# Optimization experiments

Hardware: AMD Instinct MI355X
Metric: run time of the kernel (lower is better)

The kernel has to match this reference:

```python
import jax, jax.numpy as jnp
import numpy as np

DIM = 768
HEADS = 12
E = 8
TOPK = 2
EPS = 1e-5


def layer_norm(x, g, b):
    m = jnp.mean(x, axis=-1, keepdims=True)
    v = jnp.mean((x - m) ** 2, axis=-1, keepdims=True)
    return (x - m) * jax.lax.rsqrt(v + EPS) * g + b


def setup_inputs() -> dict:
    key = jax.random.key(0)
    ks = jax.random.split(key, 12)
    B, N, C = 16, 1024, DIM
    s = 0.02
    return {
        "x": jax.random.normal(ks[0], (B, N, C), jnp.float32),
        "noise": jax.random.normal(ks[1], (B, N, E), jnp.float32),
        "ln1_g": jnp.ones((C,), jnp.float32),
        "ln1_b": jnp.zeros((C,), jnp.float32),
        "qkv_w": jax.random.normal(ks[2], (C, 3 * C), jnp.float32) * s,  # pre-transposed
        "proj_w": jax.random.normal(ks[3], (C, C), jnp.float32) * s,
        "proj_b": jnp.zeros((C,), jnp.float32),
        "ln2_g": jnp.ones((C,), jnp.float32),
        "ln2_b": jnp.zeros((C,), jnp.float32),
        "route_w": jax.random.normal(ks[4], (C, E), jnp.float32) * s,
        "route_b": jnp.zeros((E,), jnp.float32),
        "rln_g": jnp.ones((E,), jnp.float32),
        "rln_b": jnp.zeros((E,), jnp.float32),
        "expert_w": jax.random.normal(ks[5], (E, C, C), jnp.float32) * s,  # [E, in, out]
        "expert_b": jnp.zeros((E, C), jnp.float32),
    }


def reference(x, noise, ln1_g, ln1_b, qkv_w, proj_w, proj_b, ln2_g, ln2_b,
              route_w, route_b, rln_g, rln_b, expert_w, expert_b):
    B, N, C = x.shape
    H = HEADS
    Dh = C // H
    scale = Dh ** -0.5

    # --- Attention branch ---
    h = layer_norm(x, ln1_g, ln1_b)
    qkv = (h @ qkv_w).reshape(B, N, 3, H, Dh)
    q, k, v = qkv[:, :, 0], qkv[:, :, 1], qkv[:, :, 2]  # [B,N,H,Dh]
    attn = jnp.einsum('bnhd,bmhd->bhnm', q, k) * scale
    attn = jax.nn.softmax(attn, axis=-1)
    o = jnp.einsum('bhnm,bmhd->bnhd', attn, v).reshape(B, N, C)
    x = x + o @ proj_w + proj_b

    # --- MoE branch ---
    h = layer_norm(x, ln2_g, ln2_b)
    logits = layer_norm(h @ route_w + route_b, rln_g, rln_b)  # [B,N,E]
    rw = jax.nn.softmax(logits, axis=-1) + noise * (1.0 / E)
    topk_w, topk_idx = jax.lax.top_k(rw, TOPK)               # [B,N,K]
    topk_w = jax.nn.softmax(topk_w, axis=-1)

    # dense all-expert compute (faithful to source): [B,N,E,C]
    expert_out = jnp.einsum('bnc,ecd->bned', h, expert_w) + expert_b
    selected = jnp.take_along_axis(expert_out, topk_idx[..., None], axis=2)  # [B,N,K,C]
    moe = jnp.sum(selected * topk_w[..., None], axis=2)
    return x + moe
```

## Files before the change

kernel.cpp:

```cpp
#include <hip/hip_runtime.h>
#include <hip/hip_fp16.h>

typedef unsigned short u16;
typedef unsigned int u32;
typedef _Float16 f16;
typedef short bf16x8 __attribute__((ext_vector_type(8)));
typedef f16 f16x8 __attribute__((ext_vector_type(8)));
typedef float f32x4 __attribute__((ext_vector_type(4)));
typedef u32 u32x4 __attribute__((ext_vector_type(4)));

#define TOKENS 16384
#define CDIM 768
#define NEXP 8

#define QSCALE 0.18033688011112043f

__device__ __forceinline__ u16 f2b(float f) {
  u32 u = __float_as_uint(f);
  return (u16)((u + 0x7fffu + ((u >> 16) & 1u)) >> 16);
}
__device__ __forceinline__ u16 f16bits(f16 x) {
  union { f16 f; u16 u; } c;
  c.f = x;
  return c.u;
}
__device__ __forceinline__ f32x4 mfma_bf(bf16x8 a, bf16x8 b, f32x4 c) {
  return __builtin_amdgcn_mfma_f32_16x16x32_bf16(a, b, c, 0, 0, 0);
}
__device__ __forceinline__ f32x4 mfma_h(f16x8 a, f16x8 b, f32x4 c) {
  return __builtin_amdgcn_mfma_f32_16x16x32_f16(a, b, c, 0, 0, 0);
}
__device__ __forceinline__ void split8(const float* v, f16x8& h, f16x8& l) {
#pragma unroll
  for (int i = 0; i < 8; i++) {
    const f16 hh = (f16)v[i];
    h[i] = hh;
    l[i] = (f16)(v[i] - (float)hh);
  }
}

__global__ __launch_bounds__(256) void transpose_split_f16(
    const float* __restrict__ in, f16* __restrict__ oh, f16* __restrict__ ol,
    int K, int N) {
  __shared__ float tile[64][65];
  const int n0 = blockIdx.x * 64, k0 = blockIdx.y * 64;
#pragma unroll
  for (int i = 0; i < 16; i++) {
    const int s = threadIdx.x + i * 256;
    const int r = s >> 6, c = s & 63;
    tile[r][c] = in[(size_t)(k0 + r) * N + n0 + c];
  }
  __syncthreads();
#pragma unroll
  for (int i = 0; i < 16; i++) {
    const int s = threadIdx.x + i * 256;
    const int r = s >> 6, c = s & 63;
    const float v = tile[c][r];
    const f16 h = (f16)v;
    oh[(size_t)(n0 + r) * K + k0 + c] = h;
    ol[(size_t)(n0 + r) * K + k0 + c] = (f16)(v - (float)h);
  }
}

__global__ __launch_bounds__(256) void transpose_f32_bf16(
    const float* __restrict__ in, u16* __restrict__ out, int K, int N) {
  __shared__ u16 tile[64][65];
  const int z = blockIdx.z;
  in += (size_t)z * K * N;
  out += (size_t)z * K * N;
  const int n0 = blockIdx.x * 64, k0 = blockIdx.y * 64;
#pragma unroll
  for (int i = 0; i < 16; i++) {
    const int s = threadIdx.x + i * 256;
    const int r = s >> 6, c = s & 63;
    tile[r][c] = f2b(in[(size_t)(k0 + r) * N + n0 + c]);
  }
  __syncthreads();
#pragma unroll
  for (int i = 0; i < 16; i++) {
    const int s = threadIdx.x + i * 256;
    const int r = s >> 6, c = s & 63;
    out[(size_t)(n0 + r) * K + k0 + c] = tile[c][r];
  }
}

template <bool BF16OUT>
__global__ __launch_bounds__(256) void ln_rows(const float* __restrict__ in,
                                               const float* __restrict__ g,
                                               const float* __restrict__ bt,
                                               void* __restrict__ out) {
  const int row = blockIdx.x * 4 + (threadIdx.x >> 6);
  const int lane = threadIdx.x & 63;
  const size_t base = (size_t)row * CDIM;
  float v[12];
  float s = 0.f, ss = 0.f;
#pragma unroll
  for (int j = 0; j < 12; j++) {
    const int idx = lane + j * 64;
    v[j] = in[base + idx];
    s += v[j];
    ss += v[j] * v[j];
  }
#pragma unroll
  for (int m = 1; m < 64; m <<= 1) {
    s += __shfl_xor(s, m);
    ss += __shfl_xor(ss, m);
  }
  const float mean = s * (1.f / CDIM);
  const float var = ss * (1.f / CDIM) - mean * mean;
  const float rs = rsqrtf(var + 1e-5f);
#pragma unroll
  for (int j = 0; j < 12; j++) {
    const int idx = lane + j * 64;
    const float y = (v[j] - mean) * rs * g[idx] + bt[idx];
    if (BF16OUT)
      ((u16*)out)[base + idx] = f2b(y);
    else
      ((float*)out)[base + idx] = y;
  }
}

__global__ __launch_bounds__(256) void ln_rows_split(
    const float* __restrict__ in, const float* __restrict__ g,
    const float* __restrict__ bt, f16* __restrict__ oh,
    f16* __restrict__ ol) {
  const int row = blockIdx.x * 4 + (threadIdx.x >> 6);
  const int lane = threadIdx.x & 63;
  const size_t base = (size_t)row * CDIM;
  float v[12];
  float s = 0.f, ss = 0.f;
#pragma unroll
  for (int j = 0; j < 12; j++) {
    const int idx = lane + j * 64;
    v[j] = in[base + idx];
    s += v[j];
    ss += v[j] * v[j];
  }
#pragma unroll
  for (int m = 1; m < 64; m <<= 1) {
    s += __shfl_xor(s, m);
    ss += __shfl_xor(ss, m);
  }
  const float mean = s * (1.f / CDIM);
  const float var = ss * (1.f / CDIM) - mean * mean;
  const float rs = rsqrtf(var + 1e-5f);
#pragma unroll
  for (int j = 0; j < 12; j++) {
    const int idx = lane + j * 64;
    const float y = (v[j] - mean) * rs * g[idx] + bt[idx];
    const f16 hh = (f16)y;
    oh[base + idx] = hh;
    ol[base + idx] = (f16)(y - (float)hh);
  }
}

template <int EPI, bool ASPLIT>
__global__ __launch_bounds__(256) void gemm_f16s(
    const float* __restrict__ A, const f16* __restrict__ Ath,
    const f16* __restrict__ Atl, const f16* __restrict__ Bth,
    const f16* __restrict__ Btl, float* __restrict__ C, int M, int N, int K,
    const float* __restrict__ bias, const float* __restrict__ xres,
    f16* __restrict__ Oh, f16* __restrict__ Ol, u32* __restrict__ Ov) {
  __shared__ f16 Ah[128 * 64];
  __shared__ f16 Al[128 * 64];
  __shared__ f16 Bh[128 * 64];
  __shared__ f16 Bl[128 * 64];
  const int tid = threadIdx.x;
  const int lane = tid & 63, wv = tid >> 6;
  const int wr = wv >> 1, wc = wv & 1;
  const int lm = lane & 15, lq = lane >> 4;
  const int m0 = blockIdx.y * 128, n0 = blockIdx.x * 128;
  f32x4 acc[4][4];
  const f32x4 z4 = {0.f, 0.f, 0.f, 0.f};
#pragma unroll
  for (int i = 0; i < 4; i++)
#pragma unroll
    for (int j = 0; j < 4; j++) acc[i][j] = z4;

  for (int k0 = 0; k0 < K; k0 += 64) {
    __syncthreads();
#pragma unroll
    for (int i = 0; i < 4; i++) {
      const int s = tid + i * 256;
      const int r = s >> 3, g = s & 7;
      const int sw = r * 64 + ((g ^ (r & 7)) << 3);
      if constexpr (ASPLIT) {
        *(f16x8*)(&Ah[sw]) =
            *(const f16x8*)(Ath + (size_t)(m0 + r) * K + k0 + g * 8);
        *(f16x8*)(&Al[sw]) =
            *(const f16x8*)(Atl + (size_t)(m0 + r) * K + k0 + g * 8);
      } else {
        float av[8];
        *(float4*)&av[0] =
            *(const float4*)(A + (size_t)(m0 + r) * K + k0 + g * 8);
        *(float4*)&av[4] =
            *(const float4*)(A + (size_t)(m0 + r) * K + k0 + g * 8 + 4);
        f16x8 hh, ll;
        split8(av, hh, ll);
        *(f16x8*)(&Ah[sw]) = hh;
        *(f16x8*)(&Al[sw]) = ll;
      }
      *(f16x8*)(&Bh[sw]) = *(const f16x8*)(Bth + (size_t)(n0 + r) * K + k0 + g * 8);
      *(f16x8*)(&Bl[sw]) = *(const f16x8*)(Btl + (size_t)(n0 + r) * K + k0 + g * 8);
    }
    __syncthreads();
#pragma unroll
    for (int kx = 0; kx < 8; kx += 4) {
      f16x8 afh[4], afl[4], bfh[4], bfl[4];
#pragma unroll
      for (int i = 0; i < 4; i++) {
        const int ra = wr * 64 + i * 16 + lm;
        const int aw = ra * 64 + (((ra & 7) ^ (kx + lq)) << 3);
        afh[i] = *(const f16x8*)(&Ah[aw]);
        afl[i] = *(const f16x8*)(&Al[aw]);
        const int rb = wc * 64 + i * 16 + lm;
        const int bw = rb * 64 + (((rb & 7) ^ (kx + lq)) << 3);
        bfh[i] = *(const f16x8*)(&Bh[bw]);
        bfl[i] = *(const f16x8*)(&Bl[bw]);
      }
#pragma unroll
      for (int i = 0; i < 4; i++)
#pragma unroll
        for (int j = 0; j < 4; j++) {
          acc[i][j] = mfma_h(afh[i], bfh[j], acc[i][j]);
          acc[i][j] = mfma_h(afh[i], bfl[j], acc[i][j]);
          acc[i][j] = mfma_h(afl[i], bfh[j], acc[i][j]);
        }
    }
  }
#pragma unroll
  for (int i = 0; i < 4; i++)
#pragma unroll
    for (int r = 0; r < 4; r++) {
      const size_t row = m0 + wr * 64 + i * 16 + lq * 4 + r;
#pragma unroll
      for (int j = 0; j < 4; j++) {
        const int col = n0 + wc * 64 + j * 16 + lm;
        float v = acc[i][j][r];
        if constexpr (EPI == 0) {
          C[row * N + col] = v;
        } else if constexpr (EPI == 1) {
          v += bias[col] + xres[row * N + col];
          C[row * N + col] = v;
        } else {
          if (n0 < 768) v *= QSCALE;
          const f16 hh = (f16)v;
          const f16 ll = (f16)(v - (float)hh);
          if (n0 < 1536) {
            Oh[row * 1536 + col] = hh;
            Ol[row * 1536 + col] = ll;
          } else {
            Ov[row * 768 + (col - 1536)] =
                (u32)f16bits(hh) | ((u32)f16bits(ll) << 16);
          }
        }
      }
    }
}

__global__ __launch_bounds__(256) void attn_f16s(
    const f16* __restrict__ qkh, const f16* __restrict__ qkl,
    const u32* __restrict__ vI, f16* __restrict__ oh, f16* __restrict__ ol,
    int qb) {
  __shared__ f16 Kh[64 * 64];
  __shared__ f16 Kl[64 * 64];
  __shared__ f16 Vh[64 * 64];
  __shared__ f16 Vl[64 * 64];
  __shared__ f16 Ph[4 * 16 * 64];
  __shared__ f16 Pl[4 * 16 * 64];
  const int bz = blockIdx.z, h = blockIdx.y, qt = blockIdx.x;
  const int tid = threadIdx.x, wv = tid >> 6, lane = tid & 63;
  const int lm = lane & 15, lq = lane >> 4;

  f16x8 qh[2], ql[2];
  {
    const size_t qrow =
        (size_t)(bz * 1024 + qt * 64 + wv * 16 + lm) * 1536 + h * 64;
#pragma unroll
    for (int f = 0; f < 2; f++) {
      qh[f] = *(const f16x8*)(qkh + qrow + f * 32 + lq * 8);
      ql[f] = *(const f16x8*)(qkl + qrow + f * 32 + lq * 8);
    }
  }
  const f32x4 z4 = {0.f, 0.f, 0.f, 0.f};
  f32x4 oacc[4];
#pragma unroll
  for (int jb = 0; jb < 4; jb++) oacc[jb] = z4;
  float mrun[4], lrun[4];
#pragma unroll
  for (int r = 0; r < 4; r++) {
    mrun[r] = -1e30f;
    lrun[r] = 0.f;
  }
  const int vd = tid & 63;
  const int vkg = tid >> 6;
  f16* pwh = &Ph[wv * 16 * 64];
  f16* pwl = &Pl[wv * 16 * 64];

  for (int kt = 0; kt < 16; kt++) {
    __syncthreads();
#pragma unroll
    for (int i = 0; i < 2; i++) {
      const int s2 = tid + i * 256;
      const int r = s2 >> 3, g = s2 & 7;
      const size_t kb =
          (size_t)(bz * 1024 + kt * 64 + r) * 1536 + 768 + h * 64 + g * 8;
      const int sw = r * 64 + ((g ^ (r & 7)) << 3);
      *(f16x8*)(&Kh[sw]) = *(const f16x8*)(qkh + kb);
      *(f16x8*)(&Kl[sw]) = *(const f16x8*)(qkl + kb);
    }
#pragma unroll
    for (int sseg = 0; sseg < 2; sseg++) {
      const int k0v = vkg * 16 + sseg * 8;
      f16x8 hh, ll;
#pragma unroll
      for (int j = 0; j < 8; j++) {
        const u32 w = vI[(size_t)(bz * 1024 + kt * 64 + k0v + j) * 768 +
                         h * 64 + vd];
        ((u16*)&hh)[j] = (u16)(w & 0xffffu);
        ((u16*)&ll)[j] = (u16)(w >> 16);
      }
      const int g = k0v >> 3;
      const int sw = vd * 64 + ((g ^ (vd & 7)) << 3);
      *(f16x8*)(&Vh[sw]) = hh;
      *(f16x8*)(&Vl[sw]) = ll;
    }
    __syncthreads();

    f32x4 sa[4];
#pragma unroll
    for (int j = 0; j < 4; j++) sa[j] = z4;
#pragma unroll
    for (int kx = 0; kx < 8; kx += 4) {
      const f16x8 ah = qh[kx >> 2], al = ql[kx >> 2];
#pragma unroll
      for (int j = 0; j < 4; j++) {
        const int rb = j * 16 + lm;
        const int bw = rb * 64 + (((rb & 7) ^ (kx + lq)) << 3);
        const f16x8 bh = *(const f16x8*)(&Kh[bw]);
        const f16x8 bl = *(const f16x8*)(&Kl[bw]);
        sa[j] = mfma_h(ah, bh, sa[j]);
        sa[j] = mfma_h(ah, bl, sa[j]);
        sa[j] = mfma_h(al, bh, sa[j]);
      }
    }

#pragma unroll
    for (int r = 0; r < 4; r++) {
      float mx = fmaxf(fmaxf(sa[0][r], sa[1][r]), fmaxf(sa[2][r], sa[3][r]));
      mx = fmaxf(mx, __shfl_xor(mx, 1));
      mx = fmaxf(mx, __shfl_xor(mx, 2));
      mx = fmaxf(mx, __shfl_xor(mx, 4));
      mx = fmaxf(mx, __shfl_xor(mx, 8));
      const float mnew = fmaxf(mrun[r], mx);
      const float alpha = exp2f(mrun[r] - mnew);
      float ps = 0.f;
#pragma unroll
      for (int j = 0; j < 4; j++) {
        const float p = exp2f(sa[j][r] - mnew);
        sa[j][r] = p;
        ps += p;
      }
      ps += __shfl_xor(ps, 1);
      ps += __shfl_xor(ps, 2);
      ps += __shfl_xor(ps, 4);
      ps += __shfl_xor(ps, 8);
      lrun[r] = lrun[r] * alpha + ps;
      mrun[r] = mnew;
#pragma unroll
      for (int jb = 0; jb < 4; jb++) oacc[jb][r] *= alpha;
    }

#pragma unroll
    for (int j = 0; j < 4; j++)
#pragma unroll
      for (int r = 0; r < 4; r++) {
        const int qr = lq * 4 + r;
        const int key = j * 16 + lm;
        const int ad = qr * 64 + (((qr & 7) ^ (key >> 3)) << 3) + (key & 7);
        const float p = sa[j][r];
        const f16 ph = (f16)p;
        pwh[ad] = ph;
        pwl[ad] = (f16)(p - (float)ph);
      }
#pragma unroll
    for (int kx2 = 0; kx2 < 8; kx2 += 4) {
      const int pw = lm * 64 + (((lm & 7) ^ (kx2 + lq)) << 3);
      const f16x8 pah = *(const f16x8*)(&pwh[pw]);
      const f16x8 pal = *(const f16x8*)(&pwl[pw]);
#pragma unroll
      for (int jb = 0; jb < 4; jb++) {
        const int rb = jb * 16 + lm;
        const int vw = rb * 64 + (((rb & 7) ^ (kx2 + lq)) << 3);
        const f16x8 vh = *(const f16x8*)(&Vh[vw]);
        const f16x8 vl = *(const f16x8*)(&Vl[vw]);
        oacc[jb] = mfma_h(pah, vh, oacc[jb]);
        oacc[jb] = mfma_h(pah, vl, oacc[jb]);
        oacc[jb] = mfma_h(pal, vh, oacc[jb]);
      }
    }
  }
  const int gtok = (qb * 4 + bz) * 1024 + qt * 64;
#pragma unroll
  for (int r = 0; r < 4; r++) {
    const float inv = 1.f / lrun[r];
    const size_t row = (size_t)gtok + wv * 16 + lq * 4 + r;
#pragma unroll
    for (int jb = 0; jb < 4; jb++) {
      const int col = h * 64 + jb * 16 + lm;
      const float y = oacc[jb][r] * inv;
      const f16 hh = (f16)y;
      oh[row * CDIM + col] = hh;
      ol[row * CDIM + col] = (f16)(y - (float)hh);
    }
  }
}

__global__ __launch_bounds__(256) void gemm_expert(
    const u16* __restrict__ A, const u16* __restrict__ Bt,
    __half* __restrict__ Cp, int N, int K, const float* __restrict__ bias,
    const int* __restrict__ counts, const int* __restrict__ eBase,
    const int* __restrict__ tokList, const float* __restrict__ wgtList) {
  __shared__ u16 As[128 * 64];
  __shared__ u16 Bs[128 * 64];
  const int did = blockIdx.x;
  const int e = did & 7;
  const int s = did >> 3;
  const int bx = s % 6;
  const int by = s / 6;
  const int cnt = counts[e];
  const int m0 = by * 128, n0 = bx * 128;
  if (m0 >= cnt) return;
  const int tid = threadIdx.x;
  const int lane = tid & 63, wv = tid >> 6;
  const int wr = wv >> 1, wc = wv & 1;
  const int lm = lane & 15, lq = lane >> 4;
  const u16* Bte = Bt + (size_t)e * N * K;
  const int* tokl = tokList + e * TOKENS;
  const float* wl = wgtList + e * TOKENS;
  const float* biasE = bias + e * N;
  const int base0 = eBase[e];

  const int r0 = tid >> 3, g = tid & 7;
  const int swz = (g ^ (r0 & 7)) << 3;
  const u16* ap[4];
  const u16* bp[4];
#pragma unroll
  for (int i = 0; i < 4; i++) {
    const int row = m0 + r0 + i * 32;
    const int tok = (row < cnt) ? tokl[row] : 0;
    ap[i] = A + (size_t)tok * K + g * 8;
    bp[i] = Bte + (size_t)(n0 + r0 + i * 32) * K + g * 8;
  }

  f32x4 acc[4][4];
  const f32x4 z4 = {0.f, 0.f, 0.f, 0.f};
#pragma unroll
  for (int i = 0; i < 4; i++)
#pragma unroll
    for (int j = 0; j < 4; j++) acc[i][j] = z4;

  u32x4 pa[4], pb[4];
#pragma unroll
  for (int i = 0; i < 4; i++) {
    pa[i] = *(const u32x4*)(ap[i]);
    pb[i] = *(const u32x4*)(bp[i]);
  }
#pragma unroll
  for (int i = 0; i < 4; i++) {
    *(u32x4*)(&As[(r0 + i * 32) * 64 + swz]) = pa[i];
    *(u32x4*)(&Bs[(r0 + i * 32) * 64 + swz]) = pb[i];
  }

  for (int k0 = 0; k0 < K; k0 += 64) {
    __syncthreads();
    const bool more = (k0 + 64) < K;
    if (more) {
#pragma unroll
      for (int i = 0; i < 4; i++) {
        pa[i] = *(const u32x4*)(ap[i] + k0 + 64);
        pb[i] = *(const u32x4*)(bp[i] + k0 + 64);
      }
    }
#pragma unroll
    for (int kx = 0; kx < 8; kx += 4) {
      bf16x8 af[4], bfv[4];
#pragma unroll
      for (int i = 0; i < 4; i++) {
        const int ra = wr * 64 + i * 16 + lm;
        af[i] = *(const bf16x8*)(&As[ra * 64 + (((ra & 7) ^ (kx + lq)) << 3)]);
        const int rb = wc * 64 + i * 16 + lm;
        bfv[i] = *(const bf16x8*)(&Bs[rb * 64 + (((rb & 7) ^ (kx + lq)) << 3)]);
      }
#pragma unroll
      for (int i = 0; i < 4; i++)
#pragma unroll
        for (int j = 0; j < 4; j++)
          acc[i][j] = mfma_bf(af[i], bfv[j], acc[i][j]);
    }
    __syncthreads();
    if (more) {
#pragma unroll
      for (int i = 0; i < 4; i++) {
        *(u32x4*)(&As[(r0 + i * 32) * 64 + swz]) = pa[i];
        *(u32x4*)(&Bs[(r0 + i * 32) * 64 + swz]) = pb[i];
      }
    }
  }
#pragma unroll
  for (int i = 0; i < 4; i++)
#pragma unroll
    for (int r = 0; r < 4; r++) {
      const int rowi = m0 + wr * 64 + i * 16 + lq * 4 + r;
      const bool live = (rowi < cnt);
      const float w = live ? wl[rowi] : 0.f;
      const size_t prow = live ? (size_t)(base0 + rowi) * (size_t)N : 0;
#pragma unroll
      for (int j = 0; j < 4; j++) {
        const int col = n0 + wc * 64 + j * 16 + lm;
        const float v = (acc[i][j][r] + biasE[col]) * w;
        const float vn = __shfl_xor(v, 1);
        if (live && (lm & 1) == 0) {
          *(__half2*)(Cp + prow + col) =
              __halves2half2(__float2half(v), __float2half(vn));
        }
      }
    }
}

__global__ __launch_bounds__(256) void router_kernel(
    const float* __restrict__ x2, const float* __restrict__ g2,
    const float* __restrict__ b2, const float* __restrict__ rw,
    const float* __restrict__ rb, const float* __restrict__ rlng,
    const float* __restrict__ rlnb, const float* __restrict__ noise,
    int* __restrict__ eidx, float* __restrict__ ewgt) {
  const int token = blockIdx.x * 4 + (threadIdx.x >> 6);
  const int lane = threadIdx.x & 63;
  const size_t base = (size_t)token * CDIM;
  float v[12];
  float s = 0.f, ss = 0.f;
#pragma unroll
  for (int j = 0; j < 12; j++) {
    const int idx = lane + j * 64;
    v[j] = x2[base + idx];
    s += v[j];
    ss += v[j] * v[j];
  }
#pragma unroll
  for (int m = 1; m < 64; m <<= 1) {
    s += __shfl_xor(s, m);
    ss += __shfl_xor(ss, m);
  }
  const float mean = s * (1.f / CDIM);
  const float var = ss * (1.f / CDIM) - mean * mean;
  const float rs = rsqrtf(var + 1e-5f);

  float acc[8];
#pragma unroll
  for (int e = 0; e < 8; e++) acc[e] = 0.f;
#pragma unroll
  for (int j = 0; j < 12; j++) {
    const int d = lane + j * 64;
    const float hv = (v[j] - mean) * rs * g2[d] + b2[d];
    const f32x4 w0v = *(const f32x4*)(rw + (size_t)d * 8);
    const f32x4 w1v = *(const f32x4*)(rw + (size_t)d * 8 + 4);
#pragma unroll
    for (int e = 0; e < 4; e++) {
      acc[e] += hv * w0v[e];
      acc[e + 4] += hv * w1v[e];
    }
  }
#pragma unroll
  for (int m = 1; m < 64; m <<= 1)
#pragma unroll
    for (int e = 0; e < 8; e++) acc[e] += __shfl_xor(acc[e], m);

  float y[8];
  float emean = 0.f;
#pragma unroll
  for (int e = 0; e < 8; e++) {
    y[e] = acc[e] + rb[e];
    emean += y[e];
  }
  emean *= 0.125f;
  float evar = 0.f;
#pragma unroll
  for (int e = 0; e < 8; e++) {
    const float d = y[e] - emean;
    evar += d * d;
  }
  evar *= 0.125f;
  const float ers = rsqrtf(evar + 1e-5f);
  float lg[8];
  float mx = -1e30f;
#pragma unroll
  for (int e = 0; e < 8; e++) {
    lg[e] = (y[e] - emean) * ers * rlng[e] + rlnb[e];
    mx = fmaxf(mx, lg[e]);
  }
  float se = 0.f;
#pragma unroll
  for (int e = 0; e < 8; e++) {
    lg[e] = expf(lg[e] - mx);
    se += lg[e];
  }
  const float inv = 1.f / se;
  float r2[8];
#pragma unroll
  for (int e = 0; e < 8; e++)
    r2[e] = lg[e] * inv + noise[(size_t)token * 8 + e] * 0.125f;

  int e0 = 0;
  float v0 = r2[0];
#pragma unroll
  for (int e = 1; e < 8; e++)
    if (r2[e] > v0) {
      v0 = r2[e];
      e0 = e;
    }
  int e1 = -1;
  float v1 = -1e30f;
#pragma unroll
  for (int e = 0; e < 8; e++)
    if (e != e0 && r2[e] > v1) {
      v1 = r2[e];
      e1 = e;
    }
  const float w0 = 1.f / (1.f + expf(v1 - v0));
  if (lane == 0) {
    eidx[token * 2] = e0;
    eidx[token * 2 + 1] = e1;
    ewgt[token * 2] = w0;
    ewgt[token * 2 + 1] = 1.f - w0;
  }
}

__global__ __launch_bounds__(256) void build_lists(
    const int* __restrict__ eidx, const float* __restrict__ ewgt,
    int* __restrict__ counts, int* __restrict__ tokL, float* __restrict__ wgtL,
    int* __restrict__ posL) {
  const int e = blockIdx.x;
  __shared__ int cnt;
  if (threadIdx.x == 0) cnt = 0;
  __syncthreads();
  const int lane = threadIdx.x & 63;
  for (int t = threadIdx.x; t < TOKENS; t += 256) {
#pragma unroll
    for (int k = 0; k < 2; k++) {
      const bool match = (eidx[t * 2 + k] == e);
      const unsigned long long mb = __ballot(match);
      if (mb) {
        const int leader = __ffsll((unsigned long long)mb) - 1;
        int base = 0;
        if (lane == leader) base = atomicAdd(&cnt, __popcll(mb));
        base = __shfl(base, leader);
        if (match) {
          const int rank = __popcll(mb & ((1ull << lane) - 1ull));
          tokL[e * TOKENS + base + rank] = t;
          wgtL[e * TOKENS + base + rank] = ewgt[t * 2 + k];
          posL[t * 2 + k] = base + rank;
        }
      }
    }
  }
  __syncthreads();
  if (threadIdx.x == 0) counts[e] = cnt;
}

__global__ void prefix_counts(const int* __restrict__ counts,
                              int* __restrict__ eBase) {
  if (threadIdx.x == 0) {
    int s = 0;
#pragma unroll
    for (int e = 0; e < NEXP; e++) {
      eBase[e] = s;
      s += counts[e];
    }
    eBase[NEXP] = s;
  }
}

__global__ __launch_bounds__(256) void combine_moe(
    float* __restrict__ x2, const __half* __restrict__ Cp,
    const int* __restrict__ eidx, const int* __restrict__ posL,
    const int* __restrict__ eBase) {
  const int t = blockIdx.x * 4 + (threadIdx.x >> 6);
  const int lane = threadIdx.x & 63;
  const int e0 = eidx[t * 2], e1 = eidx[t * 2 + 1];
  const size_t q0 = (size_t)(eBase[e0] + posL[t * 2]) * CDIM;
  const size_t q1 = (size_t)(eBase[e1] + posL[t * 2 + 1]) * CDIM;
  const size_t base = (size_t)t * CDIM;
#pragma unroll
  for (int j = 0; j < 12; j++) {
    const int d = lane + j * 64;
    const float m =
        __half2float(Cp[q0 + d]) + __half2float(Cp[q1 + d]);
    x2[base + d] += m;
  }
}

__global__ __launch_bounds__(256) void copy_f32(const float* __restrict__ in,
                                                float* __restrict__ out) {
  const int i = (blockIdx.x * 256 + threadIdx.x) * 4;
  *(float4*)(out + i) = *(const float4*)(in + i);
}

extern "C" void kernel_launch(void* const* d_in, const int* in_sizes, int n_in,
                              void* d_out, int out_size, void* d_ws,
                              size_t ws_size, hipStream_t stream) {
  const float* x = (const float*)d_in[0];
  const float* noise = (const float*)d_in[1];
  const float* ln1_g = (const float*)d_in[2];
  const float* ln1_b = (const float*)d_in[3];
  const float* qkv_w = (const float*)d_in[4];
  const float* proj_w = (const float*)d_in[5];
  const float* proj_b = (const float*)d_in[6];
  const float* ln2_g = (const float*)d_in[7];
  const float* ln2_b = (const float*)d_in[8];
  const float* route_w = (const float*)d_in[9];
  const float* route_b = (const float*)d_in[10];
  const float* rln_g = (const float*)d_in[11];
  const float* rln_b = (const float*)d_in[12];
  const float* expert_w = (const float*)d_in[13];
  const float* expert_b = (const float*)d_in[14];

  char* ws = (char*)d_ws;
  float* x2f = (float*)(ws);
  f16* qkh = (f16*)(ws + 50331648);
  f16* qkl = (f16*)(ws + 62914560);
  u32* vIq = (u32*)(ws + 75497472);
  u16* exp_wt = (u16*)(ws + 50331648);
  u16* h2 = (u16*)(ws + 59768832);
  int* counts = (int*)(ws + 84934656);
  int* eBase = (int*)(ws + 84934784);
  int* eidx = (int*)(ws + 84934912);
  float* ewgt = (float*)(ws + 85065984);
  int* tokL = (int*)(ws + 85197056);
  float* wgtL = (float*)(ws + 85721344);
  int* posL = (int*)(ws + 86245632);
  f16* qkvw_h = (f16*)(ws + 88080384);
  f16* qkvw_l = (f16*)(ws + 91619328);
  f16* projw_h = (f16*)(ws + 95158272);
  f16* projw_l = (f16*)(ws + 96337920);
  f16* h1h = (f16*)d_out;
  f16* h1l = (f16*)((char*)d_out + 25165824);
  __half* cperm = (__half*)d_out;

  const dim3 blk(256);
  transpose_split_f16<<<dim3(36, 12), blk, 0, stream>>>(qkv_w, qkvw_h, qkvw_l,
                                                        768, 2304);
  transpose_split_f16<<<dim3(12, 12), blk, 0, stream>>>(proj_w, projw_h,
                                                        projw_l, 768, 768);
  ln_rows_split<<<dim3(4096), blk, 0, stream>>>(x, ln1_g, ln1_b, h1h, h1l);
  for (int q = 0; q < 4; q++) {
    gemm_f16s<2, true><<<dim3(18, 32), blk, 0, stream>>>(
        nullptr, h1h + (size_t)q * 4096 * 768, h1l + (size_t)q * 4096 * 768,
        qkvw_h, qkvw_l, nullptr, 4096, 2304, 768, nullptr, nullptr, qkh, qkl,
        vIq);
    attn_f16s<<<dim3(16, 12, 4), blk, 0, stream>>>(qkh, qkl, vIq, h1h, h1l,
                                                   q);
  }
  gemm_f16s<1, true><<<dim3(6, 128), blk, 0, stream>>>(
      nullptr, h1h, h1l, projw_h, projw_l, x2f, 16384, 768, 768, proj_b, x,
      nullptr, nullptr, nullptr);
  ln_rows<true><<<dim3(4096), blk, 0, stream>>>(x2f, ln2_g, ln2_b, h2);
  transpose_f32_bf16<<<dim3(12, 12, 8), blk, 0, stream>>>(expert_w, exp_wt,
                                                          768, 768);
  router_kernel<<<dim3(4096), blk, 0, stream>>>(x2f, ln2_g, ln2_b, route_w,
                                                route_b, rln_g, rln_b, noise,
                                                eidx, ewgt);
  build_lists<<<dim3(8), blk, 0, stream>>>(eidx, ewgt, counts, tokL, wgtL,
                                           posL);
  prefix_counts<<<dim3(1), dim3(64), 0, stream>>>(counts, eBase);
  gemm_expert<<<dim3(6144), blk, 0, stream>>>(h2, exp_wt, cperm, 768, 768,
                                              expert_b, counts, eBase, tokL,
                                              wgtL);
  combine_moe<<<dim3(4096), blk, 0, stream>>>(x2f, cperm, eidx, posL, eBase);
  copy_f32<<<dim3(12288), blk, 0, stream>>>(x2f, (float*)d_out);
}
```

Baseline: 1.105 ms.

## Prefetch next K/V tile into registers during attention compute

The attention kernel now issues global loads for the next K and V tile into registers before computing on the current tile. After the PV accumulation it syncs and writes the prefetched data to LDS. This hides global memory latency behind the MFMA work, at the cost of extra registers (roughly 48 more per thread), which may reduce occupancy.

```diff
diff --git a/kernel.cpp b/kernel.cpp
--- a/kernel.cpp
+++ b/kernel.cpp
@@ -297,35 +297,57 @@
   f16* pwh = &Ph[wv * 16 * 64];
   f16* pwl = &Pl[wv * 16 * 64];
 
+  const int kr0 = tid >> 3, kg = tid & 7;
+  const int ksw = (kg ^ (kr0 & 7)) << 3;
+  const size_t kbase =
+      (size_t)bz * 1024 * 1536 + 768 + (size_t)h * 64 + kg * 8;
+  const size_t vbase = (size_t)bz * 1024 * 768 + (size_t)h * 64 + vd;
+
+  f16x8 pkh[2], pkl[2];
+  u32 pv0[8], pv1[8];
+
+  auto attn_load = [&](int KT) {
+#pragma unroll
+    for (int i = 0; i < 2; i++) {
+      const size_t rr = (size_t)(KT * 64 + kr0 + i * 32) * 1536;
+      pkh[i] = *(const f16x8*)(qkh + kbase + rr);
+      pkl[i] = *(const f16x8*)(qkl + kbase + rr);
+    }
+#pragma unroll
+    for (int j = 0; j < 8; j++) {
+      pv0[j] = vI[vbase + (size_t)(KT * 64 + vkg * 16 + j) * 768];
+      pv1[j] = vI[vbase + (size_t)(KT * 64 + vkg * 16 + 8 + j) * 768];
+    }
+  };
+  auto vunpack = [&](const u32 (&pw)[8], int sseg) {
+    f16x8 hh, ll;
+#pragma unroll
+    for (int j = 0; j < 8; j++) {
+      ((u16*)&hh)[j] = (u16)(pw[j] & 0xffffu);
+      ((u16*)&ll)[j] = (u16)(pw[j] >> 16);
+    }
+    const int g = vkg * 2 + sseg;
+    const int sw = vd * 64 + ((g ^ (vd & 7)) << 3);
+    *(f16x8*)(&Vh[sw]) = hh;
+    *(f16x8*)(&Vl[sw]) = ll;
+  };
+  auto attn_write = [&]() {
+#pragma unroll
+    for (int i = 0; i < 2; i++) {
+      const int sw = (kr0 + i * 32) * 64 + ksw;
+      *(f16x8*)(&Kh[sw]) = pkh[i];
+      *(f16x8*)(&Kl[sw]) = pkl[i];
+    }
+    vunpack(pv0, 0);
+    vunpack(pv1, 1);
+  };
+
+  attn_load(0);
+  attn_write();
+
   for (int kt = 0; kt < 16; kt++) {
     __syncthreads();
-#pragma unroll
-    for (int i = 0; i < 2; i++) {
-      const int s2 = tid + i * 256;
-      const int r = s2 >> 3, g = s2 & 7;
-      const size_t kb =
-          (size_t)(bz * 1024 + kt * 64 + r) * 1536 + 768 + h * 64 + g * 8;
-      const int sw = r * 64 + ((g ^ (r & 7)) << 3);
-      *(f16x8*)(&Kh[sw]) = *(const f16x8*)(qkh + kb);
-      *(f16x8*)(&Kl[sw]) = *(const f16x8*)(qkl + kb);
-    }
-#pragma unroll
-    for (int sseg = 0; sseg < 2; sseg++) {
-      const int k0v = vkg * 16 + sseg * 8;
-      f16x8 hh, ll;
-#pragma unroll
-      for (int j = 0; j < 8; j++) {
-        const u32 w = vI[(size_t)(bz * 1024 + kt * 64 + k0v + j) * 768 +
-                         h * 64 + vd];
-        ((u16*)&hh)[j] = (u16)(w & 0xffffu);
-        ((u16*)&ll)[j] = (u16)(w >> 16);
-      }
-      const int g = k0v >> 3;
-      const int sw = vd * 64 + ((g ^ (vd & 7)) << 3);
-      *(f16x8*)(&Vh[sw]) = hh;
-      *(f16x8*)(&Vl[sw]) = ll;
-    }
-    __syncthreads();
+    if (kt + 1 < 16) attn_load(kt + 1);
 
     f32x4 sa[4];
 #pragma unroll
@@ -399,6 +421,9 @@
         oacc[jb] = mfma_h(pal, vh, oacc[jb]);
       }
     }
+
+    __syncthreads();
+    if (kt + 1 < 16) attn_write();
   }
   const int gtok = (qb * 4 + bz) * 1024 + qt * 64;
 #pragma unroll
```

After: 1.103 ms. No clear change (-0.2%).
